# Performance work log

Measured on AMD Instinct MI355X. Metric: run time of the kernel, lower is better.

The kernel has to match this reference:

```python
import jax, jax.numpy as jnp
import numpy as np

B, S, D = 4, 2048, 1024
NEG_INF = jnp.float32(-jnp.inf)


def setup_inputs() -> dict:
    key = jax.random.key(0)
    kx, kq, kk, kv = jax.random.split(key, 4)
    scale = 0.02
    return {
        "x": jax.random.normal(kx, (B, S, D), dtype=jnp.float32),
        "Wq": jax.random.normal(kq, (D, D), dtype=jnp.float32) * scale,
        "Wk": jax.random.normal(kk, (D, D), dtype=jnp.float32) * scale,
        "Wv": jax.random.normal(kv, (D, D), dtype=jnp.float32) * scale,
    }


def reference(x, Wq, Wk, Wv):
    # nn.Linear(d_in, d_out): y = x @ W.T (no bias; qkv_bias=False)
    q = jnp.einsum("bsd,ed->bse", x, Wq)
    k = jnp.einsum("bsd,ed->bse", x, Wk)
    v = jnp.einsum("bsd,ed->bse", x, Wv)
    n = x.shape[1]
    scores = jnp.einsum("bqe,bke->bqk", q, k)  # [B, S, S]
    # causal mask: positions k > q are masked with -inf
    causal = jnp.tril(jnp.ones((n, n), dtype=bool))
    scores = jnp.where(causal[None, :, :], scores, NEG_INF)
    attn = jax.nn.softmax(scores / jnp.sqrt(jnp.float32(k.shape[-1])), axis=-1)
    # dropout p=0.0 (eval) -> identity
    return jnp.einsum("bqk,bke->bqe", attn, v)
```

## Files before the change

kernel.cpp:

```cpp
#include <hip/hip_runtime.h>
#include <hip/hip_bf16.h>
#include <stdint.h>
#include <stddef.h>


typedef __hip_bfloat16 bf16;
typedef short short8 __attribute__((ext_vector_type(8)));
typedef short short4v __attribute__((ext_vector_type(4)));
typedef float f32x4 __attribute__((ext_vector_type(4)));

#define BM 128
#define BN 128
#define BK 64

__device__ __forceinline__ void cstore(float* p, float v) { *p = v; }
__device__ __forceinline__ void cstore(bf16* p, float v) { *p = __float2bfloat16(v); }

__global__ __launch_bounds__(256)
void f2b(const float* __restrict__ s, bf16* __restrict__ d, int n) {
  const int i = (blockIdx.x * 256 + threadIdx.x) * 4;
  if (i >= n) return;
  const float4 v = *(const float4*)(s + i);
  bf16 t[4] = {__float2bfloat16(v.x), __float2bfloat16(v.y),
               __float2bfloat16(v.z), __float2bfloat16(v.w)};
  *(short4v*)(d + i) = *(short4v*)t;
}

__global__ __launch_bounds__(256)
void f2b3(const float* __restrict__ a, const float* __restrict__ b,
          const float* __restrict__ c, bf16* __restrict__ d, int n) {
  const float* s = (blockIdx.y == 0) ? a : (blockIdx.y == 1) ? b : c;
  const int i = (blockIdx.x * 256 + threadIdx.x) * 4;
  if (i >= n) return;
  const float4 v = *(const float4*)(s + i);
  bf16 t[4] = {__float2bfloat16(v.x), __float2bfloat16(v.y),
               __float2bfloat16(v.z), __float2bfloat16(v.w)};
  *(short4v*)(d + (size_t)blockIdx.y * n + i) = *(short4v*)t;
}

template <typename CT>
__global__ __launch_bounds__(256, 3)
void gemm_bt(const bf16* __restrict__ A, const bf16* __restrict__ B,
             CT* __restrict__ C, int lda, int ldb, int ldc, int K,
             long sA, long sB, long sC, float scale,
             int causal_skip, int causal_klimit) {
  int by = blockIdx.y, bx = blockIdx.x;
  if (causal_klimit) by = gridDim.y - 1 - by;
  if (causal_skip && bx > by) return;

  __shared__ short8 As[8 * 128];
  __shared__ short8 Bs[8 * 128];

  const int tid = threadIdx.x;
  const int wave = tid >> 6, lane = tid & 63;
  const int wm = wave >> 1, wn = wave & 1;
  const int l15 = lane & 15, q4 = lane >> 4;
  const int bm0 = by * BM, bn0 = bx * BN;

  const bf16* Az = A + (long)blockIdx.z * sA;
  const bf16* Bz = B + (long)blockIdx.z * sB;
  CT* Cz = C + (long)blockIdx.z * sC;

  const int kg = (lane >> 3) & 7;
  const int rl = wave * 8 + (lane & 7);

  const bf16* apg = Az + (size_t)(bm0 + rl) * lda + kg * 8;
  const bf16* bpg = Bz + (size_t)(bn0 + rl) * ldb + kg * 8;
  const size_t la32 = (size_t)32 * lda, lb32 = (size_t)32 * ldb;
  short8* dstA = &As[kg * 128 + rl];
  short8* dstB = &Bs[kg * 128 + rl];

  const int Ke = causal_klimit ? min(K, (by + 1) * BM) : K;

  f32x4 acc[4][4] = {};
  short8 ra[4], rb[4];

#pragma unroll
  for (int j = 0; j < 4; j++) {
    ra[j] = *(const short8*)(apg + j * la32);
    rb[j] = *(const short8*)(bpg + j * lb32);
  }

  for (int k0 = 0; k0 < Ke; k0 += BK) {
    __syncthreads();
#pragma unroll
    for (int j = 0; j < 4; j++) {
      dstA[j * 32] = ra[j];
      dstB[j * 32] = rb[j];
    }
    __syncthreads();

    const int kn = k0 + BK;
    if (kn < Ke) {
#pragma unroll
      for (int j = 0; j < 4; j++) {
        ra[j] = *(const short8*)(apg + j * la32 + kn);
        rb[j] = *(const short8*)(bpg + j * lb32 + kn);
      }
    }

#pragma unroll
    for (int s = 0; s < 2; s++) {
      const int ch = (s * 4 + q4) * 128;
      short8 af[4], bfr[4];
#pragma unroll
      for (int i = 0; i < 4; i++)
        af[i] = As[ch + wm * 64 + i * 16 + l15];
#pragma unroll
      for (int j = 0; j < 4; j++)
        bfr[j] = Bs[ch + wn * 64 + j * 16 + l15];
#pragma unroll
      for (int i = 0; i < 4; i++)
#pragma unroll
        for (int j = 0; j < 4; j++)
          acc[i][j] = __builtin_amdgcn_mfma_f32_16x16x32_bf16(af[i], bfr[j], acc[i][j], 0, 0, 0);
    }
  }

#pragma unroll
  for (int i = 0; i < 4; i++) {
#pragma unroll
    for (int j = 0; j < 4; j++) {
#pragma unroll
      for (int r = 0; r < 4; r++) {
        const int row = bm0 + wm * 64 + i * 16 + q4 * 4 + r;
        const int col = bn0 + wn * 64 + j * 16 + l15;
        cstore(&Cz[(size_t)row * ldc + col], acc[i][j][r] * scale);
      }
    }
  }
}

__global__ __launch_bounds__(256)
void softmax_rows(const bf16* __restrict__ Sc, bf16* __restrict__ P, int S) {
  const int q = blockIdx.x, b = blockIdx.y;
  const short8* srow = (const short8*)(Sc + ((size_t)b * S + q) * S);
  short8* prow = (short8*)(P + ((size_t)b * S + q) * S);
  const int len = q + 1;
  const int tid = threadIdx.x;
  const int wave = tid >> 6, lane = tid & 63;
  __shared__ float red[10];

  const short8 raw = srow[tid];
  float v[8];
#pragma unroll
  for (int j = 0; j < 8; j++) {
    const int k = tid * 8 + j;
    const float f = __bfloat162float(((const bf16*)&raw)[j]);
    v[j] = (k < len) ? f : -1e30f;
  }

  float m = v[0];
#pragma unroll
  for (int j = 1; j < 8; j++) m = fmaxf(m, v[j]);
#pragma unroll
  for (int o = 32; o; o >>= 1) m = fmaxf(m, __shfl_down(m, o));
  if (lane == 0) red[wave] = m;
  __syncthreads();
  if (tid == 0) red[8] = fmaxf(fmaxf(red[0], red[1]), fmaxf(red[2], red[3]));
  __syncthreads();
  const float M = red[8];

  float e[8], s = 0.f;
#pragma unroll
  for (int j = 0; j < 8; j++) { e[j] = __expf(v[j] - M); s += e[j]; }
#pragma unroll
  for (int o = 32; o; o >>= 1) s += __shfl_down(s, o);
  if (lane == 0) red[4 + wave] = s;
  __syncthreads();
  if (tid == 0) red[9] = red[4] + red[5] + red[6] + red[7];
  __syncthreads();
  const float inv = 1.f / red[9];

  short8 outp;
#pragma unroll
  for (int j = 0; j < 8; j++) {
    const int k = tid * 8 + j;
    ((bf16*)&outp)[j] = __float2bfloat16((k < len) ? e[j] * inv : 0.f);
  }
  prow[tid] = outp;
}

extern "C" void kernel_launch(void* const* d_in, const int* in_sizes, int n_in,
                              void* d_out, int out_size, void* d_ws, size_t ws_size,
                              hipStream_t stream) {
  const float* x  = (const float*)d_in[0];
  const float* Wq = (const float*)d_in[1];
  const float* Wk = (const float*)d_in[2];
  const float* Wv = (const float*)d_in[3];
  float* out = (float*)d_out;

  const int Bb = 4, S = 2048, D = 1024, MS = Bb * S;

  char* ws = (char*)d_ws;
  bf16* xb = (bf16*)ws;
  bf16* wb = (bf16*)(ws + (size_t)MS * D * 2);
  bf16* Q  = (bf16*)(ws + (size_t)MS * D * 2 + 3u * D * D * 2);
  bf16* Kp = Q + (size_t)MS * D;
  bf16* VT = Kp + (size_t)MS * D;
  bf16* Sc = VT + (size_t)MS * D;
  bf16* P  = (bf16*)ws;

  dim3 blk(256);

  f2b<<<dim3(MS * D / 4 / 256), blk, 0, stream>>>(x, xb, MS * D);
  f2b3<<<dim3(D * D / 4 / 256, 3), blk, 0, stream>>>(Wq, Wk, Wv, wb, D * D);

  gemm_bt<bf16><<<dim3(D / BN, MS / BM, 2), blk, 0, stream>>>(
      xb, wb, Q, D, D, D, D, 0, (long)D * D, (long)MS * D, 1.f, 0, 0);
  gemm_bt<bf16><<<dim3(MS / BN, D / BM, 1), blk, 0, stream>>>(
      wb + 2u * D * D, xb, VT, D, D, MS, D, 0, 0, 0, 1.f, 0, 0);
  gemm_bt<bf16><<<dim3(S / BN, S / BM, Bb), blk, 0, stream>>>(
      Q, Kp, Sc, D, D, S, D,
      (long)S * D, (long)S * D, (long)S * S, 0.03125f, 1, 0);
  softmax_rows<<<dim3(S, Bb), blk, 0, stream>>>(Sc, P, S);
  gemm_bt<float><<<dim3(D / BN, S / BM, Bb), blk, 0, stream>>>(
      P, VT, out, S, MS, D, S,
      (long)S * S, (long)S, (long)S * D, 1.f, 0, 1);
}
```

Baseline: 345.5 us.

## Fuse QKV projections into one GEMM launch and compact causal score grid

Merges the Q/K projection GEMM and the transposed V projection GEMM into a single launch over 24 column tiles. The V tiles are written transposed with vectorized stores, and the Q/K tiles are routed to their buffers. The causal QK^T GEMM now launches only the 136 lower-triangular tiles per batch, decoding each tile index with a square-root computation, instead of launching a full grid whose upper blocks exit early. This removes one launch and the wasted empty blocks, but adds index arithmetic and a transposed store pattern.

After: 314.1 us. 9.1% less time.

```diff
diff --git a/kernel.cpp b/kernel.cpp
--- a/kernel.cpp
+++ b/kernel.cpp
@@ -12,6 +12,8 @@
 #define BM 128
 #define BN 128
 #define BK 64
+#define MSZ 8192
+#define DD 1024
 
 __device__ __forceinline__ void cstore(float* p, float v) { *p = v; }
 __device__ __forceinline__ void cstore(bf16* p, float v) { *p = __float2bfloat16(v); }
@@ -38,15 +40,26 @@
   *(short4v*)(d + (size_t)blockIdx.y * n + i) = *(short4v*)t;
 }
 
-template <typename CT>
+template <int MODE, typename CT>
 __global__ __launch_bounds__(256, 3)
 void gemm_bt(const bf16* __restrict__ A, const bf16* __restrict__ B,
-             CT* __restrict__ C, int lda, int ldb, int ldc, int K,
-             long sA, long sB, long sC, float scale,
-             int causal_skip, int causal_klimit) {
-  int by = blockIdx.y, bx = blockIdx.x;
-  if (causal_klimit) by = gridDim.y - 1 - by;
-  if (causal_skip && bx > by) return;
+             CT* __restrict__ C, bf16* __restrict__ C2,
+             int lda, int ldb, int ldc, int K,
+             long sA, long sB, long sC, float scale) {
+  int by, bx;
+  if (MODE == 2) {
+    const int t = blockIdx.x;
+    by = (int)((__fsqrt_rn(8.f * (float)t + 1.f) - 1.f) * 0.5f);
+    while ((by + 1) * (by + 2) / 2 <= t) by++;
+    while (by * (by + 1) / 2 > t) by--;
+    bx = t - by * (by + 1) / 2;
+  } else if (MODE == 3) {
+    by = gridDim.y - 1 - blockIdx.y;
+    bx = blockIdx.x;
+  } else {
+    by = blockIdx.y;
+    bx = blockIdx.x;
+  }
 
   __shared__ short8 As[8 * 128];
   __shared__ short8 Bs[8 * 128];
@@ -70,7 +83,7 @@
   short8* dstA = &As[kg * 128 + rl];
   short8* dstB = &Bs[kg * 128 + rl];
 
-  const int Ke = causal_klimit ? min(K, (by + 1) * BM) : K;
+  const int Ke = (MODE == 3) ? min(K, (by + 1) * BM) : K;
 
   f32x4 acc[4][4] = {};
   short8 ra[4], rb[4];
@@ -117,6 +130,27 @@
     }
   }
 
+  if (MODE == 1 && bx >= 16) {
+#pragma unroll
+    for (int i = 0; i < 4; i++) {
+#pragma unroll
+      for (int j = 0; j < 4; j++) {
+        const int rowb = bm0 + wm * 64 + i * 16 + q4 * 4;
+        const int v = (bn0 - 2048) + wn * 64 + j * 16 + l15;
+        bf16 t[4] = {__float2bfloat16(acc[i][j][0]), __float2bfloat16(acc[i][j][1]),
+                     __float2bfloat16(acc[i][j][2]), __float2bfloat16(acc[i][j][3])};
+        *(short4v*)(C2 + (size_t)v * MSZ + rowb) = *(short4v*)t;
+      }
+    }
+    return;
+  }
+
+  CT* Cb = Cz;
+  int coff = bn0;
+  if (MODE == 1) {
+    Cb = Cz + (bx >= 8 ? (size_t)MSZ * DD : 0);
+    coff = (bx & 7) * BN;
+  }
 #pragma unroll
   for (int i = 0; i < 4; i++) {
 #pragma unroll
@@ -124,8 +158,8 @@
 #pragma unroll
       for (int r = 0; r < 4; r++) {
         const int row = bm0 + wm * 64 + i * 16 + q4 * 4 + r;
-        const int col = bn0 + wn * 64 + j * 16 + l15;
-        cstore(&Cz[(size_t)row * ldc + col], acc[i][j][r] * scale);
+        const int col = coff + wn * 64 + j * 16 + l15;
+        cstore(&Cb[(size_t)row * ldc + col], acc[i][j][r] * scale);
       }
     }
   }
@@ -200,21 +234,20 @@
   bf16* VT = Kp + (size_t)MS * D;
   bf16* Sc = VT + (size_t)MS * D;
   bf16* P  = (bf16*)ws;
+  (void)Kp;
 
   dim3 blk(256);
 
   f2b<<<dim3(MS * D / 4 / 256), blk, 0, stream>>>(x, xb, MS * D);
   f2b3<<<dim3(D * D / 4 / 256, 3), blk, 0, stream>>>(Wq, Wk, Wv, wb, D * D);
 
-  gemm_bt<bf16><<<dim3(D / BN, MS / BM, 2), blk, 0, stream>>>(
-      xb, wb, Q, D, D, D, D, 0, (long)D * D, (long)MS * D, 1.f, 0, 0);
-  gemm_bt<bf16><<<dim3(MS / BN, D / BM, 1), blk, 0, stream>>>(
-      wb + 2u * D * D, xb, VT, D, D, MS, D, 0, 0, 0, 1.f, 0, 0);
-  gemm_bt<bf16><<<dim3(S / BN, S / BM, Bb), blk, 0, stream>>>(
-      Q, Kp, Sc, D, D, S, D,
-      (long)S * D, (long)S * D, (long)S * S, 0.03125f, 1, 0);
+  gemm_bt<1, bf16><<<dim3(3 * D / BN, MS / BM, 1), blk, 0, stream>>>(
+      xb, wb, Q, VT, D, D, D, D, 0, 0, 0, 1.f);
+  gemm_bt<2, bf16><<<dim3(136, 1, Bb), blk, 0, stream>>>(
+      Q, Kp, Sc, nullptr, D, D, S, D,
+      (long)S * D, (long)S * D, (long)S * S, 0.03125f);
   softmax_rows<<<dim3(S, Bb), blk, 0, stream>>>(Sc, P, S);
-  gemm_bt<float><<<dim3(D / BN, S / BM, Bb), blk, 0, stream>>>(
-      P, VT, out, S, MS, D, S,
-      (long)S * S, (long)S, (long)S * D, 1.f, 0, 1);
-}
+  gemm_bt<3, float><<<dim3(D / BN, S / BM, Bb), blk, 0, stream>>>(
+      P, VT, out, nullptr, S, MS, D, S,
+      (long)S * S, (long)S, (long)S * D, 1.f);
+}
```
